# Kernel tuning notes

Measured on AMD Instinct MI355X. Metric: run time of the kernel, lower is better.

Reference implementation:

```python
import jax, jax.numpy as jnp
import numpy as np

B, N, C, K, KS, OC = 8, 4096, 64, 20, 16, 64


def setup_inputs() -> dict:
    key = jax.random.key(0)
    ks = jax.random.split(key, 6)
    return {
        'x': jax.random.normal(ks[0], (B, 3, N), jnp.float32),
        'feature': jax.random.normal(ks[1], (B, C, N), jnp.float32),
        'kernals': jax.random.normal(ks[2], (3, KS), jnp.float32),
        'mlp_w': jax.random.normal(ks[3], (C, 7), jnp.float32) * 0.1,
        'mlp_b': jnp.zeros((C,), jnp.float32),
        'conv_w': jax.random.normal(ks[4], (OC, 2 * C * KS), jnp.float32) * 0.02,
        'conv_b': jnp.zeros((OC,), jnp.float32),
        'bn_gamma': jnp.ones((OC,), jnp.float32),
        'bn_beta': jnp.zeros((OC,), jnp.float32),
    }


def reference(x, feature, kernals, mlp_w, mlp_b, conv_w, conv_b, bn_gamma, bn_beta):
    b, _, n = x.shape
    c = feature.shape[1]
    ksz = kernals.shape[1]
    k = K
    # ---- knn on coords ----
    xt = jnp.swapaxes(x, 1, 2)                      # [B,N,3]
    inner = -2.0 * jnp.einsum('bnc,bmc->bnm', xt, xt)
    xx = jnp.sum(xt * xt, axis=-1)                  # [B,N]
    pd = -xx[:, :, None] - inner - xx[:, None, :]   # negative squared dist
    idx = jax.lax.top_k(pd, k)[1]                   # [B,N,K] nearest (incl. self)
    gather = jax.vmap(lambda pts, i: pts[i])        # per-batch gather
    # ---- geometric features ----
    x_sp = gather(xt, idx)                          # [B,N,K,3]
    x_rel = x_sp - x_sp[:, :, 0:1, :]               # [B,N,K,3]
    x_dis = jnp.linalg.norm(x_rel, axis=-1, keepdims=True)
    center = jnp.broadcast_to(x_sp[:, :, 0:1, :], x_sp.shape)
    x_feats7 = jnp.concatenate([center, x_rel, x_dis], axis=-1)  # [B,N,K,7]
    # Conv1d(7,C,1) == pointwise linear over the 7 channels
    x_feats = jnp.einsum('bnkc,oc->bnok', x_feats7, mlp_w) + mlp_b[None, None, :, None]  # [B,N,C,K]
    # ---- neighbor feature gather ----
    ft = jnp.swapaxes(feature, 1, 2)                # [B,N,C]
    sp_f = gather(ft, idx)                          # [B,N,K,C]
    spirals = jnp.concatenate([jnp.swapaxes(sp_f, 2, 3), x_feats], axis=2)  # [B,N,2C,K]
    # ---- adjacency weights ----
    one_pad = jnp.zeros((k, ksz), jnp.float32).at[0, 0].set(1.0)
    aw = jnp.einsum('bnkc,cs->bnks', x_rel, kernals) + one_pad   # [B,N,K,KS]
    aw = jnp.where(aw > 0, aw, 0.0)
    aw = aw / (jnp.sum(aw, axis=2, keepdims=True) + 1e-6)
    aw = aw * aw
    aw = aw / (jnp.sum(aw, axis=2, keepdims=True) + 1e-6)
    aw = jnp.where(aw > 0.1, aw, 0.0)
    # ---- weighted aggregation + linear ----
    agg = jnp.einsum('bnck,bnks->bncs', spirals, aw)             # [B,N,2C,KS]
    agg = agg.reshape(b, n, 2 * c * ksz)
    out = agg @ conv_w.T + conv_b                                # [B,N,OC]
    out = jnp.swapaxes(out, 1, 2)                                # [B,OC,N]
    # ---- BatchNorm1d (training-mode batch statistics, eps=1e-5) ----
    mean = jnp.mean(out, axis=(0, 2), keepdims=True)
    var = jnp.var(out, axis=(0, 2), keepdims=True)
    out = (out - mean) / jnp.sqrt(var + 1e-5)
    out = out * bn_gamma[None, :, None] + bn_beta[None, :, None]
    return out
```

## Files before the change

kernel.cpp:

```cpp
#include <hip/hip_runtime.h>
#include <cfloat>
#include <math.h>

#define NB 8
#define NPT 4096
#define NC 64
#define KNN 20
#define KSZ 16
#define BPTS 8

typedef __attribute__((ext_vector_type(8))) short short8;
typedef __attribute__((ext_vector_type(4))) float f32x4;
typedef __attribute__((ext_vector_type(2))) float f32x2;

__device__ __forceinline__ unsigned short f2bf(float f) {
  unsigned u = __float_as_uint(f);
  unsigned r = (u + 0x7fffu + ((u >> 16) & 1u)) >> 16;
  return (unsigned short)r;
}
__device__ __forceinline__ float bf2f(unsigned short h) {
  return __uint_as_float(((unsigned)h) << 16);
}

__device__ __forceinline__ f32x2 pk_fma_zw(f32x2 a, f32x2 zw) {
  f32x2 d;
  asm("v_pk_fma_f32 %0, %1, %2, %2 op_sel:[0,0,1] op_sel_hi:[1,0,1]"
      : "=v"(d) : "v"(a), "v"(zw));
  return d;
}
__device__ __forceinline__ f32x2 pk_fma_s1hi(f32x2 a, f32x2 b, f32x2 c) {
  f32x2 d;
  asm("v_pk_fma_f32 %0, %1, %2, %3 op_sel:[0,1,0] op_sel_hi:[1,1,1]"
      : "=v"(d) : "v"(a), "v"(b), "v"(c));
  return d;
}
__device__ __forceinline__ f32x2 pk_fma_s1lo(f32x2 a, f32x2 b, f32x2 c) {
  f32x2 d;
  asm("v_pk_fma_f32 %0, %1, %2, %3 op_sel:[0,0,0] op_sel_hi:[1,0,1]"
      : "=v"(d) : "v"(a), "v"(b), "v"(c));
  return d;
}

__global__ void k_pack_cw(const float* __restrict__ cw, unsigned short* __restrict__ bp) {
  int t = blockIdx.x * 256 + threadIdx.x;
  int j = t & 7, lane = (t >> 3) & 63, nt = (t >> 9) & 3, ks = t >> 11;
  int k = ks * 32 + ((lane >> 4) << 3) + j;
  int o = nt * 16 + (lane & 15);
  bp[t] = f2bf(cw[o * 2048 + k]);
}

__global__ void k_pack_cw2(const float* __restrict__ cw, const float* __restrict__ mlp_w,
                           const float* __restrict__ mlp_b, unsigned short* __restrict__ bp2) {
  int t = blockIdx.x * 256 + threadIdx.x;
  int jj = t & 7, lane = (t >> 3) & 63, nt = (t >> 9) & 3, ks2 = t >> 11;
  int k = ks2 * 32 + ((lane >> 4) << 3) + jj;
  int s = k >> 3, j = k & 7;
  int o = nt * 16 + (lane & 15);
  float acc = 0.0f;
  for (int c = 0; c < 64; ++c) {
    float coef = (j < 7) ? mlp_w[c * 7 + j] : mlp_b[c];
    acc = fmaf(cw[o * 2048 + 1024 + c * 16 + s], coef, acc);
  }
  bp2[t] = f2bf(acc);
}

__global__ void k_transpose_ft(const float* __restrict__ f, unsigned short* __restrict__ ft) {
  __shared__ float tile[64][65];
  int b = blockIdx.x >> 6;
  int n0 = (blockIdx.x & 63) * 64;
  int lane = threadIdx.x & 63;
  int rr = threadIdx.x >> 6;
#pragma unroll
  for (int c0 = 0; c0 < 64; c0 += 4) {
    int c = c0 + rr;
    tile[c][lane] = f[(b * 64 + c) * 4096 + n0 + lane];
  }
  __syncthreads();
#pragma unroll
  for (int m0 = 0; m0 < 64; m0 += 4) {
    int nn = m0 + rr;
    ft[(b * 4096 + n0 + nn) * 64 + lane] = f2bf(tile[lane][nn]);
  }
}


__device__ __noinline__ void knn_full(const float4* __restrict__ pts, int n, int lane,
                                      int g, int* __restrict__ idxOut) {
  const int M = 24;
  float4 qp = pts[n];
  float qx = qp.x, qy = qp.y, qz = qp.z;
  float v[M];
  int id[M];
#pragma unroll
  for (int r = 0; r < M; ++r) { v[r] = FLT_MAX; id[r] = 0x7fffffff; }
  for (int i = 0; i < 64; ++i) {
    int j = (i << 6) | lane;
    float4 p = pts[j];
    float dx = p.x - qx, dy = p.y - qy, dz = p.z - qz;
    float d2 = fmaf(dx, dx, fmaf(dy, dy, dz * dz));
    bool c[M];
#pragma unroll
    for (int r = 0; r < M; ++r) c[r] = d2 < v[r];
#pragma unroll
    for (int r = M - 1; r >= 1; --r) {
      v[r] = c[r - 1] ? v[r - 1] : (c[r] ? d2 : v[r]);
      id[r] = c[r - 1] ? id[r - 1] : (c[r] ? j : id[r]);
    }
    v[0] = c[0] ? d2 : v[0];
    id[0] = c[0] ? j : id[0];
  }
  unsigned long long key = ((unsigned long long)__float_as_uint(v[0]) << 32) | (unsigned)id[0];
  unsigned long long ext = ~0ull;
  for (int r = 0; r < 24; ++r) {
    unsigned long long k = key;
#pragma unroll
    for (int s = 1; s < 64; s <<= 1) {
      unsigned long long o = __shfl_xor(k, s, 64);
      k = (o < k) ? o : k;
    }
    if (lane == r) ext = k;
    if (key == k) {
#pragma unroll
      for (int q = 0; q < M - 1; ++q) { v[q] = v[q + 1]; id[q] = id[q + 1]; }
      v[M - 1] = FLT_MAX;
      id[M - 1] = 0x7fffffff;
      key = ((unsigned long long)__float_as_uint(v[0]) << 32) | (unsigned)id[0];
    }
  }
  int ei = (int)(unsigned)(ext & 0xffffffffu);
  bool al = lane < 24;
  double dv = -1.0;
  if (al) {
    float4 p = pts[ei];
    double dx = (double)p.x - (double)qx;
    double dy = (double)p.y - (double)qy;
    double dz = (double)p.z - (double)qz;
    dv = dx * dx + dy * dy + dz * dz;
  }
#pragma unroll
  for (int r = 0; r < 4; ++r) {
    double bd = al ? dv : -1.0;
    int bi = al ? ei : -1;
#pragma unroll
    for (int s = 1; s < 64; s <<= 1) {
      double od = __shfl_xor(bd, s, 64);
      int oi = __shfl_xor(bi, s, 64);
      if (od > bd || (od == bd && oi > bi)) { bd = od; bi = oi; }
    }
    if (al && ei == bi) al = false;
  }
  unsigned long long msk = __ballot(al && ei != n);
  if (al) {
    if (ei == n) {
      idxOut[g * 20] = n;
    } else {
      int pos = 1 + __popcll(msk & ((1ull << lane) - 1ull));
      idxOut[g * 20 + pos] = ei;
    }
  }
}

__launch_bounds__(1024, 2)
__global__ void k_knn(const float* __restrict__ x, int* __restrict__ idxOut) {
  __shared__ float4 pts[4096];
  int b = blockIdx.x >> 6;
  const float* xb = x + b * 3 * 4096;
  for (int i = threadIdx.x; i < 4096; i += 1024) {
    float px = xb[i], py = xb[4096 + i], pz = xb[8192 + i];
    pts[i] = make_float4(px, py, pz, fmaf(px, px, fmaf(py, py, pz * pz)));
  }
  __syncthreads();

  int lane = threadIdx.x & 63;
  int w = threadIdx.x >> 6;
  int nb = ((blockIdx.x & 63) << 6) + (w << 2);
  int gb = b * 4096 + nb;

  float4 q0 = pts[nb], q1 = pts[nb + 1], q2 = pts[nb + 2], q3 = pts[nb + 3];
  f32x2 m2x01 = {-2.0f * q0.x, -2.0f * q1.x};
  f32x2 m2y01 = {-2.0f * q0.y, -2.0f * q1.y};
  f32x2 m2z01 = {-2.0f * q0.z, -2.0f * q1.z};
  f32x2 m2x23 = {-2.0f * q2.x, -2.0f * q3.x};
  f32x2 m2y23 = {-2.0f * q2.y, -2.0f * q3.y};
  f32x2 m2z23 = {-2.0f * q2.z, -2.0f * q3.z};

  float v0 = FLT_MAX, v1 = FLT_MAX, v2 = FLT_MAX, v3 = FLT_MAX;
#pragma unroll 4
  for (int i = 0; i < 64; ++i) {
    float4 p = pts[(i << 6) | lane];
    f32x2 pxy = {p.x, p.y}, pzw = {p.z, p.w};
    f32x2 t0 = pk_fma_zw(m2z01, pzw);
    f32x2 t1 = pk_fma_zw(m2z23, pzw);
    t0 = pk_fma_s1hi(m2y01, pxy, t0);
    t1 = pk_fma_s1hi(m2y23, pxy, t1);
    t0 = pk_fma_s1lo(m2x01, pxy, t0);
    t1 = pk_fma_s1lo(m2x23, pxy, t1);
    v0 = fminf(v0, t0[0]);
    v1 = fminf(v1, t0[1]);
    v2 = fminf(v2, t1[0]);
    v3 = fminf(v3, t1[1]);
  }

#pragma unroll
  for (int k = 2; k <= 64; k <<= 1) {
#pragma unroll
    for (int j = k >> 1; j > 0; j >>= 1) {
      bool sel = ((lane & k) == 0) == ((lane & j) == 0);
      {
        float o = __shfl_xor(v0, j, 64);
        v0 = sel ? fminf(v0, o) : fmaxf(v0, o);
      }
      {
        float o = __shfl_xor(v1, j, 64);
        v1 = sel ? fminf(v1, o) : fmaxf(v1, o);
      }
      {
        float o = __shfl_xor(v2, j, 64);
        v2 = sel ? fminf(v2, o) : fmaxf(v2, o);
      }
      {
        float o = __shfl_xor(v3, j, 64);
        v3 = sel ? fminf(v3, o) : fmaxf(v3, o);
      }
    }
  }
  float T0 = __shfl(v0, 23, 64);
  float T1 = __shfl(v1, 23, 64);
  float T2 = __shfl(v2, 23, 64);
  float T3 = __shfl(v3, 23, 64);

  int ei0 = -1, ei1 = -1, ei2 = -1, ei3 = -1;
  int base0 = 0, base1 = 0, base2 = 0, base3 = 0;
  bool ovf0 = false, ovf1 = false, ovf2 = false, ovf3 = false;
#pragma unroll 2
  for (int i = 0; i < 64; ++i) {
    int j = (i << 6) | lane;
    float4 p = pts[j];
    f32x2 pxy = {p.x, p.y}, pzw = {p.z, p.w};
    f32x2 t0 = pk_fma_zw(m2z01, pzw);
    f32x2 t1 = pk_fma_zw(m2z23, pzw);
    t0 = pk_fma_s1hi(m2y01, pxy, t0);
    t1 = pk_fma_s1hi(m2y23, pxy, t1);
    t0 = pk_fma_s1lo(m2x01, pxy, t0);
    t1 = pk_fma_s1lo(m2x23, pxy, t1);
    {
      bool pred = (t0[0] <= T0);
      unsigned long long mask = __ballot(pred);
      if (mask) {
        int cnt = __popcll(mask);
        if (base0 + cnt > 63) {
          ovf0 = true;
        } else {
          int dst = pred ? (base0 + __popcll(mask & ((1ull << lane) - 1ull))) : 63;
          int got = __builtin_amdgcn_ds_permute(dst << 2, j);
          bool recv = (lane >= base0) && (lane < base0 + cnt);
          ei0 = recv ? got : ei0;
        }
        base0 += cnt;
      }
    }
    {
      bool pred = (t0[1] <= T1);
      unsigned long long mask = __ballot(pred);
      if (mask) {
        int cnt = __popcll(mask);
        if (base1 + cnt > 63) {
          ovf1 = true;
        } else {
          int dst = pred ? (base1 + __popcll(mask & ((1ull << lane) - 1ull))) : 63;
          int got = __builtin_amdgcn_ds_permute(dst << 2, j);
          bool recv = (lane >= base1) && (lane < base1 + cnt);
          ei1 = recv ? got : ei1;
        }
        base1 += cnt;
      }
    }
    {
      bool pred = (t1[0] <= T2);
      unsigned long long mask = __ballot(pred);
      if (mask) {
        int cnt = __popcll(mask);
        if (base2 + cnt > 63) {
          ovf2 = true;
        } else {
          int dst = pred ? (base2 + __popcll(mask & ((1ull << lane) - 1ull))) : 63;
          int got = __builtin_amdgcn_ds_permute(dst << 2, j);
          bool recv = (lane >= base2) && (lane < base2 + cnt);
          ei2 = recv ? got : ei2;
        }
        base2 += cnt;
      }
    }
    {
      bool pred = (t1[1] <= T3);
      unsigned long long mask = __ballot(pred);
      if (mask) {
        int cnt = __popcll(mask);
        if (base3 + cnt > 63) {
          ovf3 = true;
        } else {
          int dst = pred ? (base3 + __popcll(mask & ((1ull << lane) - 1ull))) : 63;
          int got = __builtin_amdgcn_ds_permute(dst << 2, j);
          bool recv = (lane >= base3) && (lane < base3 + cnt);
          ei3 = recv ? got : ei3;
        }
        base3 += cnt;
      }
    }
  }

  int c[4], e[4];
  c[0] = ovf0 ? 0 : base0;
  c[1] = ovf1 ? 0 : base1;
  c[2] = ovf2 ? 0 : base2;
  c[3] = ovf3 ? 0 : base3;
  e[0] = ei0;
  e[1] = ei1;
  e[2] = ei2;
  e[3] = ei3;
  int rank0 = 0, rank1 = 0, rank2 = 0, rank3 = 0;
  double dm[4];
#pragma unroll
  for (int r = 0; r < 4; ++r) {
    int e_ = (lane < c[r]) ? e[r] : 0;
    e[r] = e_;
    float4 pp = pts[e_];
    float4 qq = pts[nb + r];
    double dx = (double)pp.x - (double)qq.x;
    double dy = (double)pp.y - (double)qq.y;
    double dz = (double)pp.z - (double)qq.z;
    dm[r] = dx * dx + dy * dy + dz * dz;
  }
  int cmax = max(max(c[0], c[1]), max(c[2], c[3]));
  for (int it = 0; it < cmax; ++it) {
#pragma unroll
    for (int r = 0; r < 4; ++r) {
      int lo = __builtin_amdgcn_readlane(__double2loint(dm[r]), it);
      int hi = __builtin_amdgcn_readlane(__double2hiint(dm[r]), it);
      int ir = __builtin_amdgcn_readlane(e[r], it);
      double dr = __hiloint2double(hi, lo);
      bool less = (it < c[r]) && ((dr < dm[r]) || (dr == dm[r] && ir < e[r]));
      int inc = (lane < c[r] && less) ? 1 : 0;
      if (r == 0) rank0 += inc;
      else if (r == 1) rank1 += inc;
      else if (r == 2) rank2 += inc;
      else rank3 += inc;
    }
  }
#pragma unroll
  for (int r = 0; r < 4; ++r) {
    int rk = (r == 0) ? rank0 : (r == 1) ? rank1 : (r == 2) ? rank2 : rank3;
    bool kept = (lane < c[r]) && (rk < 20);
    bool selfk = kept && (e[r] == nb + r);
    if (__ballot(selfk) != 0ull) {
      if (kept) idxOut[(gb + r) * 20 + rk] = e[r];
    } else {
      knn_full(pts, nb + r, lane, gb + r, idxOut);
    }
  }
}

#define AGG_OFF 0
#define AWB_OFF 16384
#define FPA_OFF 24576
#define F7S_OFF 28672
#define QL_OFF  31232
#define IDX_OFF 31360
#define SMEM_SZ 33792

__launch_bounds__(256, 4)
__global__ void k_main(const float* __restrict__ x, const float* __restrict__ feat,
                       const unsigned short* __restrict__ ftT, int useFtT,
                       const float* __restrict__ kern,
                       const unsigned short* __restrict__ bpk,
                       const unsigned short* __restrict__ bpk2,
                       const float* __restrict__ conv_b, const int* __restrict__ idxIn,
                       float* __restrict__ out) {
  __shared__ __align__(16) unsigned char smem[SMEM_SZ];
  unsigned short* agg = (unsigned short*)(smem + AGG_OFF);
  unsigned short* awB = (unsigned short*)(smem + AWB_OFF);
  float4* f7s = (float4*)(smem + F7S_OFF);
  float4* qL = (float4*)(smem + QL_OFF);
  int* idxL = (int*)(smem + IDX_OFF);

  int t = threadIdx.x;
  int lane = t & 63;
  int w = t >> 6;
  int b = blockIdx.x & 7;
  int n0 = (blockIdx.x >> 3) * BPTS;
  int g0 = b * 4096 + n0;
  const float* xb = x + b * 3 * 4096;

  {
    int pt = t >> 5, slot = t & 31;
    int n = n0 + pt;
    float qx = xb[n], qy = xb[4096 + n], qz = xb[8192 + n];
    if (slot < 20) {
      int kk = idxIn[(g0 + pt) * 20 + slot];
      idxL[pt * 20 + slot] = kk;
      float rx = xb[kk] - qx, ry = xb[4096 + kk] - qy, rz = xb[8192 + kk] - qz;
      float ds = sqrtf(rx * rx + ry * ry + rz * rz);
      f7s[pt * 20 + slot] = make_float4(rx, ry, rz, ds);
    } else if (slot == 20) {
      qL[pt] = make_float4(qx, qy, qz, 0.0f);
    }
  }
  __syncthreads();

  if (t < 128) {
    int pt = t >> 4, s = t & 15;
    float kx = kern[s], ky = kern[16 + s], kz = kern[32 + s];
    float wv[20];
#pragma unroll
    for (int k = 0; k < 20; ++k) {
      float4 f = f7s[pt * 20 + k];
      float dot = f.x * kx + f.y * ky + f.z * kz;
      if (s == 0 && k == 0) dot += 1.0f;
      wv[k] = dot > 0.0f ? dot : 0.0f;
    }
    float sum = 0.0f;
#pragma unroll
    for (int k = 0; k < 20; ++k) sum += wv[k];
    float inv1 = 1.0f / (sum + 1e-6f);
    float sum2 = 0.0f;
#pragma unroll
    for (int k = 0; k < 20; ++k) {
      float u = wv[k] * inv1;
      sum2 += u * u;
    }
    float inv2 = 1.0f / (sum2 + 1e-6f);
    float colsum = 0.0f;
    float F0 = 0.0f, F1 = 0.0f, F2 = 0.0f, F3 = 0.0f;
    unsigned short* awp = awB + pt * 512;
#pragma unroll
    for (int k = 0; k < 20; ++k) {
      float u = wv[k] * inv1;
      u = u * u * inv2;
      u = (u > 0.1f) ? u : 0.0f;
      awp[(((k >> 3) * 16 + s) << 3) + (k & 7)] = f2bf(u);
      colsum += u;
      float4 f = f7s[pt * 20 + k];
      F0 = fmaf(f.x, u, F0);
      F1 = fmaf(f.y, u, F1);
      F2 = fmaf(f.z, u, F2);
      F3 = fmaf(f.w, u, F3);
    }
#pragma unroll
    for (int k = 20; k < 32; ++k)
      awp[(((k >> 3) * 16 + s) << 3) + (k & 7)] = 0;
    float4 q = qL[pt];
    __align__(16) unsigned short tmp[8];
    tmp[0] = f2bf(q.x * colsum);
    tmp[1] = f2bf(q.y * colsum);
    tmp[2] = f2bf(q.z * colsum);
    tmp[3] = f2bf(F0);
    tmp[4] = f2bf(F1);
    tmp[5] = f2bf(F2);
    tmp[6] = f2bf(F3);
    tmp[7] = f2bf(colsum);
    *(uint4*)(smem + FPA_OFF + pt * 256 + ((s ^ (pt & 7)) << 4)) = *(uint4*)tmp;
  }
  __syncthreads();

  {
    int r15 = lane & 15, chunk = lane >> 4;
#pragma unroll
    for (int half = 0; half < 2; ++half) {
      int pt = (w << 1) + half;
      int nofs[8];
#pragma unroll
      for (int j = 0; j < 8; ++j) {
        int k = (chunk << 3) + j;
        nofs[j] = (k < 20) ? ((b * 4096 + idxL[pt * 20 + k]) << 6) : -1;
      }
      short8 bfrag = *(const short8*)(awB + pt * 512 + (lane << 3));
      f32x4 accA[4];
#pragma unroll
      for (int ct = 0; ct < 4; ++ct) accA[ct] = (f32x4){0.f, 0.f, 0.f, 0.f};
#pragma unroll
      for (int ct = 0; ct < 4; ++ct) {
        int c = (ct << 4) + r15;
        union { short8 v; unsigned short u[8]; } af;
#pragma unroll
        for (int j = 0; j < 8; ++j) {
          unsigned short val = 0;
          if (nofs[j] >= 0) {
            if (useFtT) val = ftT[nofs[j] + c];
            else val = f2bf(feat[(b * 64 + c) * 4096 + (nofs[j] >> 6) - b * 4096]);
          }
          af.u[j] = val;
        }
        accA[ct] = __builtin_amdgcn_mfma_f32_16x16x32_bf16(af.v, bfrag, accA[ct], 0, 0, 0);
      }
      char* rb = (char*)(smem + AGG_OFF) + pt * 2048;
      int sw = (pt & 7) << 4;
#pragma unroll
      for (int ct = 0; ct < 4; ++ct)
#pragma unroll
        for (int q = 0; q < 4; ++q) {
          int kidx = (((ct << 4) + (chunk << 2) + q) << 4) + r15;
          *(unsigned short*)(rb + ((kidx << 1) ^ sw)) = f2bf(accA[ct][q]);
        }
    }
  }
  __syncthreads();

  f32x4 acc[4];
#pragma unroll
  for (int nt = 0; nt < 4; ++nt) acc[nt] = (f32x4){0.f, 0.f, 0.f, 0.f};
  {
    int r = lane & 15;
    const char* rowbase = (const char*)(smem + AGG_OFF) + r * 2048;
#pragma unroll
    for (int ks = 0; ks < 8; ++ks) {
      int ksl = w * 8 + ks;
      int off = (ksl * 64 + ((lane >> 4) << 4)) ^ ((r & 7) << 4);
      short8 af = *(const short8*)(rowbase + off);
#pragma unroll
      for (int nt = 0; nt < 4; ++nt) {
        short8 bf = *(const short8*)(bpk + (((ksl * 4 + nt) * 64 + lane) << 3));
        acc[nt] = __builtin_amdgcn_mfma_f32_16x16x32_bf16(af, bf, acc[nt], 0, 0, 0);
      }
    }
    {
      int chunk = (w << 2) + (lane >> 4);
      short8 af = *(const short8*)(smem + FPA_OFF + r * 256 + ((chunk ^ (r & 7)) << 4));
#pragma unroll
      for (int nt = 0; nt < 4; ++nt) {
        short8 bf = *(const short8*)(bpk2 + ((((w << 2) + nt) * 64 + lane) << 3));
        acc[nt] = __builtin_amdgcn_mfma_f32_16x16x32_bf16(af, bf, acc[nt], 0, 0, 0);
      }
    }
  }
  __syncthreads();

  float* red = (float*)(smem + AGG_OFF);
  {
#pragma unroll
    for (int nt = 0; nt < 4; ++nt)
#pragma unroll
      for (int r = 0; r < 4; ++r) {
        int row = ((lane >> 4) << 2) + r;
        if (row < 8) {
          int o = nt * 16 + (lane & 15);
          red[(w * 8 + row) * 64 + (o ^ ((row & 7) << 2))] = acc[nt][r];
        }
      }
  }
  __syncthreads();
#pragma unroll
  for (int rep = 0; rep < 2; ++rep) {
    int u = rep * 256 + t;
    int pt = u & 7, o = u >> 3;
    float s = conv_b[o];
#pragma unroll
    for (int w2 = 0; w2 < 4; ++w2) s += red[(w2 * 8 + pt) * 64 + (o ^ ((pt & 7) << 2))];
    out[(b * 64 + o) * 4096 + n0 + pt] = s;
  }
}

__global__ void k_bnstats1(const float* __restrict__ out, double* __restrict__ partial) {
  __shared__ double rs[256], rq[256];
  int o = blockIdx.x & 63, b = blockIdx.x >> 6;
  const float* p = out + (b * 64 + o) * 4096;
  double s = 0.0, q = 0.0;
  for (int i = threadIdx.x; i < 4096; i += 256) {
    double v = (double)p[i];
    s += v;
    q += v * v;
  }
  rs[threadIdx.x] = s;
  rq[threadIdx.x] = q;
  __syncthreads();
  for (int st = 128; st > 0; st >>= 1) {
    if ((int)threadIdx.x < st) {
      rs[threadIdx.x] += rs[threadIdx.x + st];
      rq[threadIdx.x] += rq[threadIdx.x + st];
    }
    __syncthreads();
  }
  if (threadIdx.x == 0) {
    partial[(o * 8 + b) * 2] = rs[0];
    partial[(o * 8 + b) * 2 + 1] = rq[0];
  }
}

__global__ void k_bnstats2(const double* __restrict__ partial, const float* __restrict__ gamma,
                           const float* __restrict__ beta, float* __restrict__ stats) {
  int o = threadIdx.x;
  double s = 0.0, q = 0.0;
#pragma unroll
  for (int b = 0; b < 8; ++b) {
    s += partial[(o * 8 + b) * 2];
    q += partial[(o * 8 + b) * 2 + 1];
  }
  double mean = s / 32768.0;
  double var = q / 32768.0 - mean * mean;
  double inv = 1.0 / sqrt(var + 1e-5);
  double sc = (double)gamma[o] * inv;
  stats[o * 2] = (float)sc;
  stats[o * 2 + 1] = (float)((double)beta[o] - mean * sc);
}

__global__ void k_bnapply(float* __restrict__ out, const float* __restrict__ stats) {
  int i4 = blockIdx.x * 256 + threadIdx.x;
  int o = (i4 >> 10) & 63;
  float sc = stats[o * 2], sh = stats[o * 2 + 1];
  float4 v = ((const float4*)out)[i4];
  v.x = fmaf(v.x, sc, sh);
  v.y = fmaf(v.y, sc, sh);
  v.z = fmaf(v.z, sc, sh);
  v.w = fmaf(v.w, sc, sh);
  ((float4*)out)[i4] = v;
}

extern "C" void kernel_launch(void* const* d_in, const int* in_sizes, int n_in,
                              void* d_out, int out_size, void* d_ws, size_t ws_size,
                              hipStream_t stream) {
  const float* x = (const float*)d_in[0];
  const float* feat = (const float*)d_in[1];
  const float* kern = (const float*)d_in[2];
  const float* mlp_w = (const float*)d_in[3];
  const float* mlp_b = (const float*)d_in[4];
  const float* conv_w = (const float*)d_in[5];
  const float* conv_b = (const float*)d_in[6];
  const float* gamma = (const float*)d_in[7];
  const float* beta = (const float*)d_in[8];
  float* out = (float*)d_out;
  char* ws = (char*)d_ws;

  int* idx = (int*)ws;
  double* partial = (double*)(ws + 2621440);
  float* stats = (float*)(ws + 2629632);
  unsigned short* bpk = (unsigned short*)(ws + 2633728);
  unsigned short* bpk2 = (unsigned short*)(ws + 2764800);
  unsigned short* ftT = (unsigned short*)(ws + 2781184);
  int useFtT = (ws_size >= (size_t)(2781184 + 4194304)) ? 1 : 0;

  k_pack_cw<<<256, 256, 0, stream>>>(conv_w, bpk);
  k_pack_cw2<<<32, 256, 0, stream>>>(conv_w, mlp_w, mlp_b, bpk2);
  if (useFtT) k_transpose_ft<<<512, 256, 0, stream>>>(feat, ftT);
  k_knn<<<512, 1024, 0, stream>>>(x, idx);
  k_main<<<4096, 256, 0, stream>>>(x, feat, ftT, useFtT, kern, bpk, bpk2,
                                   conv_b, idx, out);
  k_bnstats1<<<512, 256, 0, stream>>>(out, partial);
  k_bnstats2<<<1, 64, 0, stream>>>(partial, gamma, beta, stats);
  k_bnapply<<<2048, 256, 0, stream>>>(out, stats);
}
```

Measured before the change: 180.3 us.

## Merge prep kernels, fold BN stats into apply, use LDS candidate lists in kNN

Merges the three weight and feature prep kernels into a single launch, and folds the BN finalize step into the apply kernel, so two separate launches are removed. In kNN, candidate indices are now compacted into a per-row shared-memory list instead of being shuffled across lanes with ds_permute, which also lets a full 64-candidate list count as non-overflowing. The transpose is now always launched, regardless of the workspace-size check. The LDS list adds 8KB of shared memory per kNN block, which may affect occupancy under the 1024x2 launch bounds.

```diff
diff --git a/kernel.cpp b/kernel.cpp
--- a/kernel.cpp
+++ b/kernel.cpp
@@ -41,45 +41,47 @@
   return d;
 }
 
-__global__ void k_pack_cw(const float* __restrict__ cw, unsigned short* __restrict__ bp) {
-  int t = blockIdx.x * 256 + threadIdx.x;
-  int j = t & 7, lane = (t >> 3) & 63, nt = (t >> 9) & 3, ks = t >> 11;
-  int k = ks * 32 + ((lane >> 4) << 3) + j;
-  int o = nt * 16 + (lane & 15);
-  bp[t] = f2bf(cw[o * 2048 + k]);
-}
-
-__global__ void k_pack_cw2(const float* __restrict__ cw, const float* __restrict__ mlp_w,
-                           const float* __restrict__ mlp_b, unsigned short* __restrict__ bp2) {
-  int t = blockIdx.x * 256 + threadIdx.x;
-  int jj = t & 7, lane = (t >> 3) & 63, nt = (t >> 9) & 3, ks2 = t >> 11;
-  int k = ks2 * 32 + ((lane >> 4) << 3) + jj;
-  int s = k >> 3, j = k & 7;
-  int o = nt * 16 + (lane & 15);
-  float acc = 0.0f;
-  for (int c = 0; c < 64; ++c) {
-    float coef = (j < 7) ? mlp_w[c * 7 + j] : mlp_b[c];
-    acc = fmaf(cw[o * 2048 + 1024 + c * 16 + s], coef, acc);
-  }
-  bp2[t] = f2bf(acc);
-}
-
-__global__ void k_transpose_ft(const float* __restrict__ f, unsigned short* __restrict__ ft) {
+__global__ void k_prep(const float* __restrict__ cw, const float* __restrict__ mlp_w,
+                       const float* __restrict__ mlp_b, const float* __restrict__ f,
+                       unsigned short* __restrict__ bp, unsigned short* __restrict__ bp2,
+                       unsigned short* __restrict__ ft) {
   __shared__ float tile[64][65];
-  int b = blockIdx.x >> 6;
-  int n0 = (blockIdx.x & 63) * 64;
-  int lane = threadIdx.x & 63;
-  int rr = threadIdx.x >> 6;
-#pragma unroll
-  for (int c0 = 0; c0 < 64; c0 += 4) {
-    int c = c0 + rr;
-    tile[c][lane] = f[(b * 64 + c) * 4096 + n0 + lane];
-  }
-  __syncthreads();
-#pragma unroll
-  for (int m0 = 0; m0 < 64; m0 += 4) {
-    int nn = m0 + rr;
-    ft[(b * 4096 + n0 + nn) * 64 + lane] = f2bf(tile[lane][nn]);
+  int blk = blockIdx.x;
+  if (blk < 256) {
+    int t = blk * 256 + threadIdx.x;
+    int j = t & 7, lane = (t >> 3) & 63, nt = (t >> 9) & 3, ks = t >> 11;
+    int k = ks * 32 + ((lane >> 4) << 3) + j;
+    int o = nt * 16 + (lane & 15);
+    bp[t] = f2bf(cw[o * 2048 + k]);
+  } else if (blk < 288) {
+    int t = (blk - 256) * 256 + threadIdx.x;
+    int jj = t & 7, lane = (t >> 3) & 63, nt = (t >> 9) & 3, ks2 = t >> 11;
+    int k = ks2 * 32 + ((lane >> 4) << 3) + jj;
+    int s = k >> 3, j = k & 7;
+    int o = nt * 16 + (lane & 15);
+    float acc = 0.0f;
+    for (int c = 0; c < 64; ++c) {
+      float coef = (j < 7) ? mlp_w[c * 7 + j] : mlp_b[c];
+      acc = fmaf(cw[o * 2048 + 1024 + c * 16 + s], coef, acc);
+    }
+    bp2[t] = f2bf(acc);
+  } else {
+    int blk3 = blk - 288;
+    int b = blk3 >> 6;
+    int n0 = (blk3 & 63) * 64;
+    int lane = threadIdx.x & 63;
+    int rr = threadIdx.x >> 6;
+#pragma unroll
+    for (int c0 = 0; c0 < 64; c0 += 4) {
+      int c = c0 + rr;
+      tile[c][lane] = f[(b * 64 + c) * 4096 + n0 + lane];
+    }
+    __syncthreads();
+#pragma unroll
+    for (int m0 = 0; m0 < 64; m0 += 4) {
+      int nn = m0 + rr;
+      ft[(b * 4096 + n0 + nn) * 64 + lane] = f2bf(tile[lane][nn]);
+    }
   }
 }
 
@@ -163,6 +165,7 @@
 __launch_bounds__(1024, 2)
 __global__ void k_knn(const float* __restrict__ x, int* __restrict__ idxOut) {
   __shared__ float4 pts[4096];
+  __shared__ unsigned short listL[64 * 64];
   int b = blockIdx.x >> 6;
   const float* xb = x + b * 3 * 4096;
   for (int i = threadIdx.x; i < 4096; i += 1024) {
@@ -173,7 +176,8 @@
 
   int lane = threadIdx.x & 63;
   int w = threadIdx.x >> 6;
-  int nb = ((blockIdx.x & 63) << 6) + (w << 2);
+  int row = w << 2;
+  int nb = ((blockIdx.x & 63) << 6) + row;
   int gb = b * 4096 + nb;
 
   float4 q0 = pts[nb], q1 = pts[nb + 1], q2 = pts[nb + 2], q3 = pts[nb + 3];
@@ -229,7 +233,6 @@
   float T2 = __shfl(v2, 23, 64);
   float T3 = __shfl(v3, 23, 64);
 
-  int ei0 = -1, ei1 = -1, ei2 = -1, ei3 = -1;
   int base0 = 0, base1 = 0, base2 = 0, base3 = 0;
   bool ovf0 = false, ovf1 = false, ovf2 = false, ovf3 = false;
 #pragma unroll 2
@@ -248,13 +251,11 @@
       unsigned long long mask = __ballot(pred);
       if (mask) {
         int cnt = __popcll(mask);
-        if (base0 + cnt > 63) {
+        if (base0 + cnt > 64) {
           ovf0 = true;
-        } else {
-          int dst = pred ? (base0 + __popcll(mask & ((1ull << lane) - 1ull))) : 63;
-          int got = __builtin_amdgcn_ds_permute(dst << 2, j);
-          bool recv = (lane >= base0) && (lane < base0 + cnt);
-          ei0 = recv ? got : ei0;
+        } else if (pred) {
+          int dst = base0 + __popcll(mask & ((1ull << lane) - 1ull));
+          listL[(row << 6) + dst] = (unsigned short)j;
         }
         base0 += cnt;
       }
@@ -264,13 +265,11 @@
       unsigned long long mask = __ballot(pred);
       if (mask) {
         int cnt = __popcll(mask);
-        if (base1 + cnt > 63) {
+        if (base1 + cnt > 64) {
           ovf1 = true;
-        } else {
-          int dst = pred ? (base1 + __popcll(mask & ((1ull << lane) - 1ull))) : 63;
-          int got = __builtin_amdgcn_ds_permute(dst << 2, j);
-          bool recv = (lane >= base1) && (lane < base1 + cnt);
-          ei1 = recv ? got : ei1;
+        } else if (pred) {
+          int dst = base1 + __popcll(mask & ((1ull << lane) - 1ull));
+          listL[((row + 1) << 6) + dst] = (unsigned short)j;
         }
         base1 += cnt;
       }
@@ -280,13 +279,11 @@
       unsigned long long mask = __ballot(pred);
       if (mask) {
         int cnt = __popcll(mask);
-        if (base2 + cnt > 63) {
+        if (base2 + cnt > 64) {
           ovf2 = true;
-        } else {
-          int dst = pred ? (base2 + __popcll(mask & ((1ull << lane) - 1ull))) : 63;
-          int got = __builtin_amdgcn_ds_permute(dst << 2, j);
-          bool recv = (lane >= base2) && (lane < base2 + cnt);
-          ei2 = recv ? got : ei2;
+        } else if (pred) {
+          int dst = base2 + __popcll(mask & ((1ull << lane) - 1ull));
+          listL[((row + 2) << 6) + dst] = (unsigned short)j;
         }
         base2 += cnt;
       }
@@ -296,13 +293,11 @@
       unsigned long long mask = __ballot(pred);
       if (mask) {
         int cnt = __popcll(mask);
-        if (base3 + cnt > 63) {
+        if (base3 + cnt > 64) {
           ovf3 = true;
-        } else {
-          int dst = pred ? (base3 + __popcll(mask & ((1ull << lane) - 1ull))) : 63;
-          int got = __builtin_amdgcn_ds_permute(dst << 2, j);
-          bool recv = (lane >= base3) && (lane < base3 + cnt);
-          ei3 = recv ? got : ei3;
+        } else if (pred) {
+          int dst = base3 + __popcll(mask & ((1ull << lane) - 1ull));
+          listL[((row + 3) << 6) + dst] = (unsigned short)j;
         }
         base3 += cnt;
       }
@@ -314,15 +309,11 @@
   c[1] = ovf1 ? 0 : base1;
   c[2] = ovf2 ? 0 : base2;
   c[3] = ovf3 ? 0 : base3;
-  e[0] = ei0;
-  e[1] = ei1;
-  e[2] = ei2;
-  e[3] = ei3;
   int rank0 = 0, rank1 = 0, rank2 = 0, rank3 = 0;
   double dm[4];
 #pragma unroll
   for (int r = 0; r < 4; ++r) {
-    int e_ = (lane < c[r]) ? e[r] : 0;
+    int e_ = (lane < c[r]) ? (int)listL[((row + r) << 6) + lane] : 0;
     e[r] = e_;
     float4 pp = pts[e_];
     float4 qq = pts[nb + r];
@@ -585,27 +576,27 @@
   }
 }
 
-__global__ void k_bnstats2(const double* __restrict__ partial, const float* __restrict__ gamma,
-                           const float* __restrict__ beta, float* __restrict__ stats) {
-  int o = threadIdx.x;
-  double s = 0.0, q = 0.0;
-#pragma unroll
-  for (int b = 0; b < 8; ++b) {
-    s += partial[(o * 8 + b) * 2];
-    q += partial[(o * 8 + b) * 2 + 1];
-  }
-  double mean = s / 32768.0;
-  double var = q / 32768.0 - mean * mean;
-  double inv = 1.0 / sqrt(var + 1e-5);
-  double sc = (double)gamma[o] * inv;
-  stats[o * 2] = (float)sc;
-  stats[o * 2 + 1] = (float)((double)beta[o] - mean * sc);
-}
-
-__global__ void k_bnapply(float* __restrict__ out, const float* __restrict__ stats) {
+__global__ void k_bnapply(float* __restrict__ out, const double* __restrict__ partial,
+                          const float* __restrict__ gamma, const float* __restrict__ beta) {
+  __shared__ float sc_sh[2];
+  int o = (blockIdx.x >> 2) & 63;
+  if (threadIdx.x == 0) {
+    double s = 0.0, q = 0.0;
+#pragma unroll
+    for (int b = 0; b < 8; ++b) {
+      s += partial[(o * 8 + b) * 2];
+      q += partial[(o * 8 + b) * 2 + 1];
+    }
+    double mean = s / 32768.0;
+    double var = q / 32768.0 - mean * mean;
+    double inv = 1.0 / sqrt(var + 1e-5);
+    double sc = (double)gamma[o] * inv;
+    sc_sh[0] = (float)sc;
+    sc_sh[1] = (float)((double)beta[o] - mean * sc);
+  }
+  __syncthreads();
   int i4 = blockIdx.x * 256 + threadIdx.x;
-  int o = (i4 >> 10) & 63;
-  float sc = stats[o * 2], sh = stats[o * 2 + 1];
+  float sc = sc_sh[0], sh = sc_sh[1];
   float4 v = ((const float4*)out)[i4];
   v.x = fmaf(v.x, sc, sh);
   v.y = fmaf(v.y, sc, sh);
@@ -631,19 +622,15 @@
 
   int* idx = (int*)ws;
   double* partial = (double*)(ws + 2621440);
-  float* stats = (float*)(ws + 2629632);
   unsigned short* bpk = (unsigned short*)(ws + 2633728);
   unsigned short* bpk2 = (unsigned short*)(ws + 2764800);
   unsigned short* ftT = (unsigned short*)(ws + 2781184);
   int useFtT = (ws_size >= (size_t)(2781184 + 4194304)) ? 1 : 0;
 
-  k_pack_cw<<<256, 256, 0, stream>>>(conv_w, bpk);
-  k_pack_cw2<<<32, 256, 0, stream>>>(conv_w, mlp_w, mlp_b, bpk2);
-  if (useFtT) k_transpose_ft<<<512, 256, 0, stream>>>(feat, ftT);
+  k_prep<<<800, 256, 0, stream>>>(conv_w, mlp_w, mlp_b, feat, bpk, bpk2, ftT);
   k_knn<<<512, 1024, 0, stream>>>(x, idx);
   k_main<<<4096, 256, 0, stream>>>(x, feat, ftT, useFtT, kern, bpk, bpk2,
                                    conv_b, idx, out);
   k_bnstats1<<<512, 256, 0, stream>>>(out, partial);
-  k_bnstats2<<<1, 64, 0, stream>>>(partial, gamma, beta, stats);
-  k_bnapply<<<2048, 256, 0, stream>>>(out, stats);
-}
+  k_bnapply<<<2048, 256, 0, stream>>>(out, partial, gamma, beta);
+}
```

After: 181.7 us. No clear change (+0.8%).
